# Kernel optimization log

Measured on AMD Instinct MI355X. Metric: run time of the kernel, lower is better.

Reference implementation:

```python
import jax, jax.numpy as jnp
import numpy as np

NEG_INF = -(2.0**32) + 1.0  # matches tf: -2**32 + 1


def _positional_encoding(seq_len, d_model):
    # sinusoidal PE exactly as in the module (sin on even cols, cos on odd cols)
    pos = np.arange(seq_len)[:, None].astype(np.float32)
    i = np.arange(d_model)[None, :]
    angle_rates = 1.0 / np.power(10000.0, 2 * (i // 2) / np.float32(d_model))
    ang = pos * angle_rates
    ang[:, 0::2] = np.sin(ang[:, 0::2])
    ang[:, 1::2] = np.cos(ang[:, 1::2])
    return jnp.asarray(ang[None, ...], dtype=jnp.float32)  # [1, S, D]


def setup_inputs() -> dict:
    key = jax.random.key(0)
    kq, kk, kv, kw, km = jax.random.split(key, 5)
    B, S, D = 64, 512, 256
    q = jax.random.normal(kq, (B, S, D), dtype=jnp.float32)
    k = jax.random.normal(kk, (B, S, D), dtype=jnp.float32)
    v = jax.random.normal(kv, (B, S, D), dtype=jnp.float32)
    # keras 'random_uniform' initializer default range is [-0.05, 0.05]
    W = jax.random.uniform(kw, (D, D), dtype=jnp.float32, minval=-0.05, maxval=0.05)
    mask = jax.random.randint(km, (B, S), 0, 2, dtype=jnp.int32)
    return {"q": q, "k": k, "v": v, "W": W, "mask": mask}


def reference(q, k, v, W, mask):
    B, S, D = q.shape
    pe = _positional_encoding(S, D)  # [1, S, D]
    q = q + pe
    k = k + pe
    q = jax.nn.relu(jnp.einsum('bsd,de->bse', q, W))
    k = jax.nn.relu(jnp.einsum('bsd,de->bse', k, W))
    logits = jnp.einsum('bqd,bkd->bqk', q, k) / jnp.sqrt(jnp.float32(D))  # [B,S,S]
    # mask over key positions, broadcast across query dim
    logits = jnp.where(mask[:, None, :] == 0, jnp.float32(NEG_INF), logits)
    att = jax.nn.softmax(logits, axis=-1)
    out = jnp.einsum('bqk,bkd->bqd', att, v)
    return jnp.mean(out, axis=1)  # [B, D]
```

## Files before the change

kernel.cpp:

```cpp
#include <hip/hip_runtime.h>

#define NEG_INF (-4294967295.0f)

typedef _Float16 f16;
typedef _Float16 f16x8 __attribute__((ext_vector_type(8)));
typedef _Float16 f16x4v __attribute__((ext_vector_type(4)));
typedef float f32x4 __attribute__((ext_vector_type(4)));

#define MFMA16(a,b,c) __builtin_amdgcn_mfma_f32_16x16x32_f16((a),(b),(c),0,0,0)

#if defined(__has_builtin)
#if __has_builtin(__builtin_amdgcn_global_load_lds)
#define HAS_GLD 1
#endif
#endif

__device__ __forceinline__ void stage16(const void* g, void* lds_base, int lane) {
#ifdef HAS_GLD
    __builtin_amdgcn_global_load_lds(
        (const __attribute__((address_space(1))) unsigned int*)g,
        (__attribute__((address_space(3))) unsigned int*)lds_base, 16, 0, 0);
#else
    ((f16x8*)lds_base)[lane] = *(const f16x8*)g;
#endif
}

__global__ __launch_bounds__(256) void pe_kernel(float* __restrict__ pe) {
    int idx = blockIdx.x * 256 + threadIdx.x;
    int s = idx >> 8, d = idx & 255;
    float x = (float)(d & ~1) * (1.f / 256.f);
    float rate = exp2f(x * -13.287712379549449f);
    float ang = (float)s * rate;
    pe[idx] = (d & 1) ? cosf(ang) : sinf(ang);
}

__global__ __launch_bounds__(256) void wt_kernel(const float* __restrict__ W,
                                                 f16* __restrict__ WT) {
    int e = blockIdx.x, d = threadIdx.x;
    WT[(e << 8) + d] = (f16)W[(d << 8) + e];
}

__global__ __launch_bounds__(256) void proj_kernel(const float* __restrict__ q,
                                                   const float* __restrict__ k,
                                                   const f16* __restrict__ WT,
                                                   const float* __restrict__ pe,
                                                   f16* __restrict__ outp) {
    __shared__ __align__(16) f16 As[2][64 * 64];
    __shared__ __align__(16) f16 WTs[2][256 * 64];
    const int t = threadIdx.x, l = t & 63, wv = t >> 6, lr = l & 15, lg = l >> 4;
    const int r0 = blockIdx.x * 64;
    const float* src = (r0 < 32768) ? q : k;
    const int rb = r0 & 32767;

    float4 av[4], pv[4];
    auto loadA = [&](int kc) {
        #pragma unroll
        for (int it = 0; it < 4; ++it) {
            int r = it * 16 + (t >> 4), d = (t & 15) * 4;
            av[it] = *(const float4*)(src + (size_t)(rb + r) * 256 + kc * 64 + d);
            pv[it] = *(const float4*)(pe + ((rb + r) & 511) * 256 + kc * 64 + d);
        }
    };
    auto writeA = [&](int dst) {
        #pragma unroll
        for (int it = 0; it < 4; ++it) {
            int r = it * 16 + (t >> 4), d = (t & 15) * 4;
            f16x4v h;
            h[0] = (f16)(av[it].x + pv[it].x); h[1] = (f16)(av[it].y + pv[it].y);
            h[2] = (f16)(av[it].z + pv[it].z); h[3] = (f16)(av[it].w + pv[it].w);
            *(f16x4v*)&As[dst][(r << 6) + (d ^ ((r & 7) << 3))] = h;
        }
    };
    auto stageW = [&](int dst, int kc) {
        #pragma unroll
        for (int it = 0; it < 8; ++it) {
            int eb = wv * 64 + it * 8;
            int e = eb + (l >> 3), c = l & 7;
            const f16* s = WT + (e << 8) + kc * 64 + ((c ^ (e & 7)) << 3);
            stage16(s, &WTs[dst][eb << 6], l);
        }
    };

    f32x4 acc[16] = {};
    loadA(0); stageW(0, 0); writeA(0);
    __syncthreads();

    for (int kc = 0; kc < 4; ++kc) {
        int cur = kc & 1;
        if (kc < 3) { loadA(kc + 1); stageW(cur ^ 1, kc + 1); }
        #pragma unroll
        for (int kk = 0; kk < 2; ++kk) {
            int dk = kk * 32 + lg * 8;
            f16x8 a = *(const f16x8*)&As[cur][((wv * 16 + lr) << 6) + (dk ^ ((lr & 7) << 3))];
            #pragma unroll
            for (int nt = 0; nt < 16; ++nt) {
                int e = nt * 16 + lr;
                f16x8 b = *(const f16x8*)&WTs[cur][(e << 6) + (dk ^ ((lr & 7) << 3))];
                acc[nt] = MFMA16(a, b, acc[nt]);
            }
        }
        if (kc < 3) { writeA(cur ^ 1); __syncthreads(); }
    }

    f16* Rb = &WTs[0][0] + wv * 4096;
    #pragma unroll
    for (int nt = 0; nt < 16; ++nt) {
        #pragma unroll
        for (int rg = 0; rg < 4; ++rg) {
            int rr = lg * 4 + rg, col = nt * 16 + lr;
            float v = acc[nt][rg];
            v = v > 0.f ? v * 0.25f : 0.f;
            Rb[rr * 256 + ((((col >> 3) ^ (rr & 7)) << 3) | (col & 7))] = (f16)v;
        }
    }
    #pragma unroll
    for (int it = 0; it < 8; ++it) {
        int row = it * 2 + (l >> 5), c = l & 31;
        f16x8 v8 = *(const f16x8*)&Rb[row * 256 + ((c ^ (row & 7)) << 3)];
        *(f16x8*)(outp + (((size_t)(r0 + wv * 16 + row)) << 8) + c * 8) = v8;
    }
}

__global__ __launch_bounds__(256) void attn_kernel(const f16* __restrict__ QP,
                                                   const f16* __restrict__ KP,
                                                   const int* __restrict__ mask,
                                                   float* __restrict__ wglob) {
    __shared__ __align__(16) f16 Ks[2][32 * 256];
    __shared__ float ws[4][512];
    const int t = threadIdx.x, l = t & 63, wv = t >> 6, lr = l & 15, lg = l >> 4;
    const int n = blockIdx.x, bb = n & 63, qt = n >> 6;
    const int q0 = qt * 64 + wv * 16;
    const int* maskb = mask + bb * 512;

    auto stageK = [&](int dst, int kt) {
        #pragma unroll
        for (int it = 0; it < 4; ++it) {
            int r2 = wv * 8 + it * 2;
            int r = r2 + (l >> 5), c = l & 31;
            const f16* s = KP + (((size_t)(bb * 512 + kt * 32 + r)) << 8) + ((c ^ (r & 7)) << 3);
            stage16(s, &Ks[dst][r2 << 8], l);
        }
    };

    f16x8 qf[8];
    const f16* qrow = QP + (((size_t)(bb * 512 + q0 + lr)) << 8);
    #pragma unroll
    for (int kk = 0; kk < 8; ++kk) qf[kk] = *(const f16x8*)(qrow + kk * 32 + lg * 8);

    unsigned mb0 = 0, mb1 = 0;
    #pragma unroll
    for (int kt = 0; kt < 16; ++kt) {
        mb0 |= (maskb[kt * 32 + lr] ? 1u : 0u) << kt;
        mb1 |= (maskb[kt * 32 + 16 + lr] ? 1u : 0u) << kt;
    }

    float lacc[4] = {0.f, 0.f, 0.f, 0.f};
    f16 Pst[16][8];

    stageK(0, 0);
    __syncthreads();

    #pragma unroll
    for (int kt = 0; kt < 16; ++kt) {
        const int cur = kt & 1;
        if (kt < 15) stageK(cur ^ 1, kt + 1);
        f32x4 s0 = {}, s1 = {};
        #pragma unroll
        for (int kk = 0; kk < 8; ++kk) {
            int dk = kk * 32 + lg * 8;
            f16x8 b0 = *(const f16x8*)&Ks[cur][(lr << 8) + (dk ^ ((lr & 7) << 3))];
            f16x8 b1 = *(const f16x8*)&Ks[cur][((16 + lr) << 8) + (dk ^ ((lr & 7) << 3))];
            s0 = MFMA16(qf[kk], b0, s0);
            s1 = MFMA16(qf[kk], b1, s1);
        }
        #pragma unroll
        for (int rg = 0; rg < 4; ++rg) {
            float p0 = __expf(((mb0 >> kt) & 1) ? s0[rg] : NEG_INF);
            float p1 = __expf(((mb1 >> kt) & 1) ? s1[rg] : NEG_INF);
            f16 h0 = (f16)p0, h1 = (f16)p1;
            Pst[kt][rg] = h0;
            Pst[kt][4 + rg] = h1;
            lacc[rg] += (float)h0 + (float)h1;
        }
        if (kt < 15) __syncthreads();
    }

    #pragma unroll
    for (int rg = 0; rg < 4; ++rg) {
        float s = lacc[rg];
        s += __shfl_xor(s, 1); s += __shfl_xor(s, 2);
        s += __shfl_xor(s, 4); s += __shfl_xor(s, 8);
        lacc[rg] = s;
    }
    float rl[4];
    float bsum = 0.f;
    #pragma unroll
    for (int rg = 0; rg < 4; ++rg) {
        if (lacc[rg] > 0.f) { rl[rg] = 1.0f / lacc[rg]; }
        else                { rl[rg] = 0.f; bsum += 1.f / 512.f; }
    }

    #pragma unroll
    for (int kt = 0; kt < 16; ++kt) {
        float w0 = (float)Pst[kt][0] * rl[0] + (float)Pst[kt][1] * rl[1]
                 + (float)Pst[kt][2] * rl[2] + (float)Pst[kt][3] * rl[3] + bsum;
        float w1 = (float)Pst[kt][4] * rl[0] + (float)Pst[kt][5] * rl[1]
                 + (float)Pst[kt][6] * rl[2] + (float)Pst[kt][7] * rl[3] + bsum;
        w0 += __shfl_xor(w0, 16); w0 += __shfl_xor(w0, 32);
        w1 += __shfl_xor(w1, 16); w1 += __shfl_xor(w1, 32);
        if (lg == 0) {
            ws[wv][kt * 32 + lr] = w0;
            ws[wv][kt * 32 + 16 + lr] = w1;
        }
    }
    __syncthreads();
    #pragma unroll
    for (int i = 0; i < 2; ++i) {
        int kk = t + i * 256;
        float s = ws[0][kk] + ws[1][kk] + ws[2][kk] + ws[3][kk];
        atomicAdd(&wglob[bb * 512 + kk], s);
    }
}

__global__ __launch_bounds__(256) void wv_kernel(const float* __restrict__ wglob,
                                                 const float* __restrict__ V,
                                                 float* __restrict__ out) {
    const int n = blockIdx.x, bb = n & 63, ks = n >> 6;
    const int d = threadIdx.x;
    const float* wr = wglob + bb * 512 + ks * 64;
    const float* vb = V + ((((size_t)bb) * 512 + ks * 64) << 8) + d;
    float acc = 0.f;
    #pragma unroll 8
    for (int kk = 0; kk < 64; ++kk) acc = fmaf(wr[kk], vb[(size_t)kk << 8], acc);
    atomicAdd(&out[bb * 256 + d], acc * (1.f / 512.f));
}

extern "C" void kernel_launch(void* const* d_in, const int* in_sizes, int n_in,
                              void* d_out, int out_size, void* d_ws, size_t ws_size,
                              hipStream_t stream) {
    const float* q  = (const float*)d_in[0];
    const float* k  = (const float*)d_in[1];
    const float* v  = (const float*)d_in[2];
    const float* W  = (const float*)d_in[3];
    const int* mask = (const int*)d_in[4];

    char* ws = (char*)d_ws;
    f16*   QP = (f16*)ws;
    f16*   KP = (f16*)(ws + 16777216);
    float* PE = (float*)(ws + 33554432);
    f16*   WT = (f16*)(ws + 34078720);
    float* WG = (float*)(ws + 34209792);

    pe_kernel<<<512, 256, 0, stream>>>(PE);
    wt_kernel<<<256, 256, 0, stream>>>(W, WT);
    proj_kernel<<<1024, 256, 0, stream>>>(q, k, WT, PE, QP);
    (void)hipMemsetAsync(WG, 0, 64 * 512 * sizeof(float), stream);
    (void)hipMemsetAsync(d_out, 0, 64 * 256 * sizeof(float), stream);
    attn_kernel<<<512, 256, 0, stream>>>(QP, KP, mask, WG);
    wv_kernel<<<512, 256, 0, stream>>>(WG, v, (float*)d_out);
}
```

Before: 179.8 us.

## Merge setup kernels and memsets, enlarge projection blocks to share W tiles

Folds the positional-encoding, W-transpose and two memsets into one setup kernel, cutting launches and memset calls. The projection kernel moves to 1024-thread blocks covering 256 rows, so each W tile staged in LDS is shared by 16 waves instead of 4 and the per-block W staging is split across them. This uses 128KB of LDS per block, which limits occupancy to one block per CU, and the grid shrinks to 256 blocks.

```diff
diff --git a/kernel.cpp b/kernel.cpp
--- a/kernel.cpp
+++ b/kernel.cpp
@@ -25,30 +25,44 @@
 #endif
 }
 
-__global__ __launch_bounds__(256) void pe_kernel(float* __restrict__ pe) {
-    int idx = blockIdx.x * 256 + threadIdx.x;
-    int s = idx >> 8, d = idx & 255;
-    float x = (float)(d & ~1) * (1.f / 256.f);
-    float rate = exp2f(x * -13.287712379549449f);
-    float ang = (float)s * rate;
-    pe[idx] = (d & 1) ? cosf(ang) : sinf(ang);
-}
-
-__global__ __launch_bounds__(256) void wt_kernel(const float* __restrict__ W,
-                                                 f16* __restrict__ WT) {
-    int e = blockIdx.x, d = threadIdx.x;
-    WT[(e << 8) + d] = (f16)W[(d << 8) + e];
-}
-
-__global__ __launch_bounds__(256) void proj_kernel(const float* __restrict__ q,
-                                                   const float* __restrict__ k,
-                                                   const f16* __restrict__ WT,
-                                                   const float* __restrict__ pe,
-                                                   f16* __restrict__ outp) {
-    __shared__ __align__(16) f16 As[2][64 * 64];
-    __shared__ __align__(16) f16 WTs[2][256 * 64];
+__global__ __launch_bounds__(256) void setup_kernel(const float* __restrict__ W,
+                                                    float* __restrict__ pe,
+                                                    f16* __restrict__ WT,
+                                                    float* __restrict__ WG,
+                                                    float* __restrict__ out) {
+    const int bid = blockIdx.x, t = threadIdx.x;
+    if (bid < 512) {
+        int idx = bid * 256 + t;
+        int s = idx >> 8, d = idx & 255;
+        float x = (float)(d & ~1) * (1.f / 256.f);
+        float rate = exp2f(x * -13.287712379549449f);
+        float ang = (float)s * rate;
+        pe[idx] = (d & 1) ? cosf(ang) : sinf(ang);
+    } else if (bid < 768) {
+        int e = bid - 512, d = t;
+        WT[(e << 8) + d] = (f16)W[(d << 8) + e];
+    } else if (bid == 768) {
+        #pragma unroll
+        for (int i = 0; i < 128; ++i) WG[i * 256 + t] = 0.f;
+    } else {
+        #pragma unroll
+        for (int i = 0; i < 64; ++i) out[i * 256 + t] = 0.f;
+    }
+}
+
+__global__ __launch_bounds__(1024, 4) void proj_kernel(const float* __restrict__ q,
+                                                       const float* __restrict__ k,
+                                                       const f16* __restrict__ WT,
+                                                       const float* __restrict__ pe,
+                                                       f16* __restrict__ outp) {
+    __shared__ __align__(16) f16 lds[65536];
+    f16* const As0 = lds;
+    f16* const As1 = lds + 16384;
+    f16* const Ws0 = lds + 32768;
+    f16* const Ws1 = lds + 49152;
+
     const int t = threadIdx.x, l = t & 63, wv = t >> 6, lr = l & 15, lg = l >> 4;
-    const int r0 = blockIdx.x * 64;
+    const int r0 = blockIdx.x * 256;
     const float* src = (r0 < 32768) ? q : k;
     const int rb = r0 & 32767;
 
@@ -56,53 +70,58 @@
     auto loadA = [&](int kc) {
         #pragma unroll
         for (int it = 0; it < 4; ++it) {
-            int r = it * 16 + (t >> 4), d = (t & 15) * 4;
+            int r = it * 64 + (t >> 4), d = (t & 15) * 4;
             av[it] = *(const float4*)(src + (size_t)(rb + r) * 256 + kc * 64 + d);
             pv[it] = *(const float4*)(pe + ((rb + r) & 511) * 256 + kc * 64 + d);
         }
     };
-    auto writeA = [&](int dst) {
+    auto writeA = [&](f16* dst) {
         #pragma unroll
         for (int it = 0; it < 4; ++it) {
-            int r = it * 16 + (t >> 4), d = (t & 15) * 4;
+            int r = it * 64 + (t >> 4), d = (t & 15) * 4;
             f16x4v h;
             h[0] = (f16)(av[it].x + pv[it].x); h[1] = (f16)(av[it].y + pv[it].y);
             h[2] = (f16)(av[it].z + pv[it].z); h[3] = (f16)(av[it].w + pv[it].w);
-            *(f16x4v*)&As[dst][(r << 6) + (d ^ ((r & 7) << 3))] = h;
-        }
-    };
-    auto stageW = [&](int dst, int kc) {
-        #pragma unroll
-        for (int it = 0; it < 8; ++it) {
-            int eb = wv * 64 + it * 8;
+            *(f16x4v*)&dst[(r << 6) + (d ^ ((r & 7) << 3))] = h;
+        }
+    };
+    auto stageW = [&](f16* dst, int kc) {
+        #pragma unroll
+        for (int it = 0; it < 2; ++it) {
+            int eb = wv * 16 + it * 8;
             int e = eb + (l >> 3), c = l & 7;
             const f16* s = WT + (e << 8) + kc * 64 + ((c ^ (e & 7)) << 3);
-            stage16(s, &WTs[dst][eb << 6], l);
+            stage16(s, &dst[eb << 6], l);
         }
     };
 
     f32x4 acc[16] = {};
-    loadA(0); stageW(0, 0); writeA(0);
-    __syncthreads();
-
+    loadA(0); stageW(Ws0, 0); writeA(As0);
+    __syncthreads();
+
+    #pragma unroll
     for (int kc = 0; kc < 4; ++kc) {
-        int cur = kc & 1;
-        if (kc < 3) { loadA(kc + 1); stageW(cur ^ 1, kc + 1); }
+        f16* const Ac = (kc & 1) ? As1 : As0;
+        f16* const Wc = (kc & 1) ? Ws1 : Ws0;
+        f16* const An = (kc & 1) ? As0 : As1;
+        f16* const Wn = (kc & 1) ? Ws0 : Ws1;
+        if (kc < 3) { loadA(kc + 1); stageW(Wn, kc + 1); }
         #pragma unroll
         for (int kk = 0; kk < 2; ++kk) {
             int dk = kk * 32 + lg * 8;
-            f16x8 a = *(const f16x8*)&As[cur][((wv * 16 + lr) << 6) + (dk ^ ((lr & 7) << 3))];
+            f16x8 a = *(const f16x8*)&Ac[((wv * 16 + lr) << 6) + (dk ^ ((lr & 7) << 3))];
             #pragma unroll
             for (int nt = 0; nt < 16; ++nt) {
                 int e = nt * 16 + lr;
-                f16x8 b = *(const f16x8*)&WTs[cur][(e << 6) + (dk ^ ((lr & 7) << 3))];
+                f16x8 b = *(const f16x8*)&Wc[(e << 6) + (dk ^ ((lr & 7) << 3))];
                 acc[nt] = MFMA16(a, b, acc[nt]);
             }
         }
-        if (kc < 3) { writeA(cur ^ 1); __syncthreads(); }
-    }
-
-    f16* Rb = &WTs[0][0] + wv * 4096;
+        if (kc < 3) { writeA(An); __syncthreads(); }
+    }
+
+    __syncthreads();
+    f16* Rb = lds + wv * 4096;
     #pragma unroll
     for (int nt = 0; nt < 16; ++nt) {
         #pragma unroll
@@ -251,11 +270,8 @@
     f16*   WT = (f16*)(ws + 34078720);
     float* WG = (float*)(ws + 34209792);
 
-    pe_kernel<<<512, 256, 0, stream>>>(PE);
-    wt_kernel<<<256, 256, 0, stream>>>(W, WT);
-    proj_kernel<<<1024, 256, 0, stream>>>(q, k, WT, PE, QP);
-    (void)hipMemsetAsync(WG, 0, 64 * 512 * sizeof(float), stream);
-    (void)hipMemsetAsync(d_out, 0, 64 * 256 * sizeof(float), stream);
+    setup_kernel<<<770, 256, 0, stream>>>(W, PE, WT, WG, (float*)d_out);
+    proj_kernel<<<256, 1024, 0, stream>>>(q, k, WT, PE, QP);
     attn_kernel<<<512, 256, 0, stream>>>(QP, KP, mask, WG);
     wv_kernel<<<512, 256, 0, stream>>>(WG, v, (float*)d_out);
 }
```

Result: faster. 175.9 us (-2.2%).
